# Optimization experiments

Hardware: AMD Instinct MI355X
Metric: run time of the kernel (lower is better)

Reference implementation:

```python
import jax, jax.numpy as jnp
import numpy as np

EPS = 1e-5  # BatchNorm2d default eps


def _conv3x3(x, w):
    # x: [B,C,H,W], w: [O,I,3,3], stride 1, padding 1, no bias
    return jax.lax.conv_general_dilated(
        x, w, window_strides=(1, 1), padding=((1, 1), (1, 1)),
        dimension_numbers=("NCHW", "OIHW", "NCHW"))


def setup_inputs() -> dict:
    key = jax.random.key(0)
    k1, k2, k3 = jax.random.split(key, 3)
    B, C, H, W = 4, 64, 24, 24
    x = jax.random.normal(k1, (B, C, H, W), dtype=jnp.float32)
    gamma = jnp.ones((C,), dtype=jnp.float32)
    beta = jnp.zeros((C,), dtype=jnp.float32)
    # fan-based init scale as in the custom Conv2d (scale=1 and scale=1e-6)
    fan_qkv = (C + 3 * C) / 2 * 9
    bound_qkv = np.sqrt(3.0 / fan_qkv)
    w_qkv = jax.random.uniform(k2, (3 * C, C, 3, 3), minval=-bound_qkv,
                               maxval=bound_qkv, dtype=jnp.float32)
    fan_out = (C + C) / 2 * 9
    bound_out = np.sqrt(3.0 * 1e-6 / fan_out)
    w_out = jax.random.uniform(k3, (C, C, 3, 3), minval=-bound_out,
                               maxval=bound_out, dtype=jnp.float32)
    return {"x": x, "gamma": gamma, "beta": beta, "w_qkv": w_qkv, "w_out": w_out}


def reference(x, gamma, beta, w_qkv, w_out):
    B, C, H, W = x.shape
    # BatchNorm2d (training-mode batch statistics, biased variance)
    mean = jnp.mean(x, axis=(0, 2, 3), keepdims=True)
    var = jnp.var(x, axis=(0, 2, 3), keepdims=True)
    xn = (x - mean) * jax.lax.rsqrt(var + EPS)
    xn = xn * gamma[None, :, None, None] + beta[None, :, None, None]
    qkv = _conv3x3(xn, w_qkv)            # [B,3C,H,W]
    q, k, v = jnp.split(qkv, 3, axis=1)  # each [B,C,H,W]
    scale = 1.0 / np.sqrt(C)
    # per-channel attention: head_dim=1, heads=C
    logits = jnp.einsum("bcyx,bchw->bcyxhw", q, k) * scale  # [B,C,H,W,H,W]
    attn = jax.nn.softmax(logits.reshape(B, C, H, W, H * W), axis=-1)
    attn = attn.reshape(B, C, H, W, H, W)
    out_v = jnp.einsum("bcyxhw,bchw->bcyx", attn, v)  # [B,C,H,W]
    return x + _conv3x3(out_v, w_out)
```

## Files before the change

kernel.cpp:

```cpp
#include <hip/hip_runtime.h>
#include <math.h>

#define B_SZ 4
#define C_IN 64
#define HW_ 576
#define PPLANE 728
#define XH_N   (B_SZ * 32 * PPLANE)

typedef _Float16 h2 __attribute__((ext_vector_type(2)));
typedef _Float16 h8 __attribute__((ext_vector_type(8)));

static __device__ __forceinline__ float dot2(h2 a, h2 b, float c) {
#if __has_builtin(__builtin_amdgcn_fdot2)
  return __builtin_amdgcn_fdot2(a, b, c, false);
#else
  return c + (float)a.x * (float)b.x + (float)a.y * (float)b.y;
#endif
}

static __device__ __forceinline__ float frcp(float d) {
#if __has_builtin(__builtin_amdgcn_rcpf)
  return __builtin_amdgcn_rcpf(d);
#else
  return 1.0f / d;
#endif
}

__global__ __launch_bounds__(256)
void stats_pack_kernel(const float* __restrict__ x, const float* __restrict__ gamma,
                       const float* __restrict__ beta, h2* __restrict__ xh) {
  const int bid = blockIdx.x, tid = threadIdx.x;
  const int icp = bid & 31, b = bid >> 5;
  __shared__ float rs[4], rss[4], ab[4];
  const int c = icp * 2 + (tid >> 7);
  float s = 0.f, ss = 0.f;
  for (int i = (tid & 127); i < B_SZ * HW_; i += 128) {
    int b2 = i / HW_, px = i - b2 * HW_;
    float v = x[(b2 * C_IN + c) * HW_ + px];
    s += v; ss = fmaf(v, v, ss);
  }
#pragma unroll
  for (int off = 32; off > 0; off >>= 1) {
    s += __shfl_down(s, off); ss += __shfl_down(ss, off);
  }
  if ((tid & 63) == 0) { rs[tid >> 6] = s; rss[tid >> 6] = ss; }
  __syncthreads();
  if (tid < 2) {
    float S = rs[tid * 2] + rs[tid * 2 + 1], SS = rss[tid * 2] + rss[tid * 2 + 1];
    const float inv_n = 1.f / (B_SZ * HW_);
    float mean = S * inv_n;
    float var  = SS * inv_n - mean * mean;
    float a = rsqrtf(var + 1e-5f) * gamma[icp * 2 + tid];
    ab[tid * 2] = a;
    ab[tid * 2 + 1] = fmaf(-mean, a, beta[icp * 2 + tid]);
  }
  __syncthreads();
  const float a0 = ab[0], b0 = ab[1], a1 = ab[2], b1 = ab[3];
  h2* plane = xh + (size_t)(b * 32 + icp) * PPLANE;
  const float* src0 = x + (size_t)(b * C_IN + icp * 2) * HW_;
  for (int e = tid; e < PPLANE; e += 256) {
    int rrow = e / 28, ecol = e - rrow * 28;
    int yy = rrow - 1, xx = ecol - 1;
    float f0 = 0.f, f1 = 0.f;
    if ((unsigned)yy < 24u && (unsigned)xx < 24u) {
      f0 = fmaf(src0[yy * 24 + xx],       a0, b0);
      f1 = fmaf(src0[HW_ + yy * 24 + xx], a1, b1);
    }
    h2 v; v.x = (_Float16)f0; v.y = (_Float16)f1;
    plane[e] = v;
  }
}

__global__ __launch_bounds__(576)
void qkv_attn_kernel(const h2* __restrict__ xh, const float* __restrict__ wq,
                     h2* __restrict__ outv) {
  const int bid = blockIdx.x, tid = threadIdx.x;
  const int b = bid >> 6, c = bid & 63;
  const int sub = tid / 144;
  const int r = tid - sub * 144;
  const int y = r / 6, x0 = (r % 6) * 4;

  __shared__ __align__(16) char smem[43424];
  h2*    Wl  = (h2*)smem;
  float* cb  = (float*)(smem + 4096);
  float2* kvs = (float2*)(smem + 24832);
  float* qs  = (float*)(smem + 29440);
  float* red = (float*)(smem + 31744);
  float* FGf = (float*)(smem + 31824);
  float* red2 = (float*)(smem + 31904);

  for (int j = tid; j < 864; j += 576) {
    int icp = j / 27, rem = j - icp * 27;
    int o = rem / 9, t = rem - o * 9;
    int oc = c + 64 * o;
    h2 v;
    v.x = (_Float16)wq[(oc * C_IN + 2 * icp) * 9 + t];
    v.y = (_Float16)wq[(oc * C_IN + 2 * icp + 1) * 9 + t];
    Wl[icp * 32 + rem] = v;
  }
  __syncthreads();

  float acc[3][4] = {{0.f,0.f,0.f,0.f},{0.f,0.f,0.f,0.f},{0.f,0.f,0.f,0.f}};
  const int icp0 = sub * 8;
  const h2* dbase = xh + ((size_t)(b * 32 + icp0) * PPLANE + y * 28 + x0);
#pragma unroll
  for (int i = 0; i < 8; ++i) {
    const h2* dp = dbase + i * PPLANE;
    union { h8 v8[2]; h2 v2[8]; } R0, R1, R2;
    R0.v8[0] = *(const h8*)(dp);      R0.v8[1] = *(const h8*)(dp + 4);
    R1.v8[0] = *(const h8*)(dp + 28); R1.v8[1] = *(const h8*)(dp + 32);
    R2.v8[0] = *(const h8*)(dp + 56); R2.v8[1] = *(const h8*)(dp + 60);
    const h2* wrow = Wl + (icp0 + i) * 32;
    union { h8 v8[7]; h2 v2[28]; } W;
#pragma unroll
    for (int j8 = 0; j8 < 7; ++j8) W.v8[j8] = *(const h8*)(wrow + j8 * 4);
#pragma unroll
    for (int o = 0; o < 3; ++o) {
#pragma unroll
      for (int p = 0; p < 4; ++p) {
        float a = acc[o][p];
        a = dot2(R0.v2[p + 0], W.v2[o * 9 + 0], a);
        a = dot2(R0.v2[p + 1], W.v2[o * 9 + 1], a);
        a = dot2(R0.v2[p + 2], W.v2[o * 9 + 2], a);
        a = dot2(R1.v2[p + 0], W.v2[o * 9 + 3], a);
        a = dot2(R1.v2[p + 1], W.v2[o * 9 + 4], a);
        a = dot2(R1.v2[p + 2], W.v2[o * 9 + 5], a);
        a = dot2(R2.v2[p + 0], W.v2[o * 9 + 6], a);
        a = dot2(R2.v2[p + 1], W.v2[o * 9 + 7], a);
        a = dot2(R2.v2[p + 2], W.v2[o * 9 + 8], a);
        acc[o][p] = a;
      }
    }
  }
  __syncthreads();
  if (sub != 0) {
    const int base = (sub - 1) * 3 * 576;
#pragma unroll
    for (int o = 0; o < 3; ++o)
#pragma unroll
      for (int p = 0; p < 4; ++p)
        cb[base + o * 576 + r * 4 + p] = acc[o][p];
  }
  __syncthreads();
  const float scale_l2e = 0.125f * 1.44269504088896341f;
  if (sub == 0) {
#pragma unroll
    for (int p = 0; p < 4; ++p) {
      float qv = acc[0][p] + cb[0 * 576 + r * 4 + p]
               + cb[3 * 576 + r * 4 + p] + cb[6 * 576 + r * 4 + p];
      float kv = acc[1][p] + cb[1 * 576 + r * 4 + p]
               + cb[4 * 576 + r * 4 + p] + cb[7 * 576 + r * 4 + p];
      float vv = acc[2][p] + cb[2 * 576 + r * 4 + p]
               + cb[5 * 576 + r * 4 + p] + cb[8 * 576 + r * 4 + p];
      qs[4 * r + p] = qv * scale_l2e;
      kvs[4 * r + p] = make_float2(kv, vv);
    }
  }
  __syncthreads();

  const float s = qs[tid];
  float smax = s, smin = s;
#pragma unroll
  for (int off = 32; off > 0; off >>= 1) {
    smax = fmaxf(smax, __shfl_down(smax, off));
    smin = fminf(smin, __shfl_down(smin, off));
  }
  const int wid = tid >> 6;
  if ((tid & 63) == 0) { red[wid] = smax; red[10 + wid] = smin; }
  __syncthreads();
  smax = red[0]; smin = red[10];
#pragma unroll
  for (int w = 1; w < 9; ++w) {
    smax = fmaxf(smax, red[w]); smin = fminf(smin, red[10 + w]);
  }
  const float cc = 0.5f * (smax + smin);
  const float rr = fmaxf(0.5f * (smax - smin), 1e-6f);
  const float COS[9] = { 0.98480775f,  0.86602540f,  0.64278761f,  0.34202014f, 0.f,
                        -0.34202014f, -0.64278761f, -0.86602540f, -0.98480775f };
  const float WJ[9]  = { 0.17364818f, -0.5f,  0.76604444f, -0.93969262f, 1.f,
                        -0.93969262f, 0.76604444f, -0.5f, 0.17364818f };
  float xj[9];
#pragma unroll
  for (int j = 0; j < 9; ++j) xj[j] = fmaf(rr, COS[j], cc);

  const float kk = kvs[tid].x, vv = kvs[tid].y;
  float fj[9], gj[9];
#pragma unroll
  for (int j = 0; j < 9; ++j) {
    float E = __builtin_amdgcn_exp2f(xj[j] * kk);
    gj[j] = E; fj[j] = E * vv;
  }
#pragma unroll
  for (int j = 0; j < 9; ++j) {
    fj[j] += __shfl_xor(fj[j], 1); gj[j] += __shfl_xor(gj[j], 1);
    fj[j] += __shfl_xor(fj[j], 2); gj[j] += __shfl_xor(gj[j], 2);
  }
  if ((tid & 3) == 0) {
    const int row = tid >> 2;
#pragma unroll
    for (int j = 0; j < 9; ++j) {
      red2[row * 20 + j] = fj[j];
      red2[row * 20 + 9 + j] = gj[j];
    }
  }
  __syncthreads();
  if (tid < 144) {
    const int j = tid >> 3, chunk = tid & 7;
    float sum = 0.f;
#pragma unroll
    for (int i = 0; i < 18; ++i) sum += red2[(chunk + 8 * i) * 20 + j];
    sum += __shfl_xor(sum, 1);
    sum += __shfl_xor(sum, 2);
    sum += __shfl_xor(sum, 4);
    if (chunk == 0) FGf[j] = sum;
  }
  __syncthreads();

  float num = 0.f, den = 0.f;
#pragma unroll
  for (int j = 0; j < 9; ++j) {
    float d = s - xj[j];
    d = copysignf(fmaxf(fabsf(d), 1e-7f), d);
    float mu = WJ[j] * frcp(d);
    num = fmaf(mu, FGf[j], num);
    den = fmaf(mu, FGf[9 + j], den);
  }
  float outval = num / den;

  const int icp = c >> 1, hc = c & 1;
  _Float16* plane = reinterpret_cast<_Float16*>(outv + ((size_t)(b * 32) + icp) * PPLANE);
  const int yy = tid / 24, xx = tid - yy * 24;
  plane[((yy + 1) * 28 + (xx + 1)) * 2 + hc] = (_Float16)outval;
  if (tid < 100) {
    int rrow, e;
    if (tid < 26)      { rrow = 0;            e = tid; }
    else if (tid < 52) { rrow = 25;           e = tid - 26; }
    else if (tid < 76) { rrow = tid - 52 + 1; e = 0; }
    else               { rrow = tid - 76 + 1; e = 25; }
    plane[(rrow * 28 + e) * 2 + hc] = (_Float16)0.f;
  }
}

__global__ __launch_bounds__(576)
void conv_out_kernel(const h2* __restrict__ outv, const float* __restrict__ wo,
                     const float* __restrict__ x, float* __restrict__ out) {
  const int bid = blockIdx.x, tid = threadIdx.x;
  const int b = bid >> 6, oc = bid & 63;
  const int sub = tid / 144;
  const int r = tid - sub * 144;
  const int y = r / 6, x0 = (r % 6) * 4;

  __shared__ __align__(16) char smem[8960];
  h2*    Wl = (h2*)smem;
  float* cb = (float*)(smem + 2048);

  for (int j = tid; j < 288; j += 576) {
    int icp = j / 9, t = j - icp * 9;
    h2 v;
    v.x = (_Float16)(wo[(oc * C_IN + 2 * icp) * 9 + t] * 4096.f);
    v.y = (_Float16)(wo[(oc * C_IN + 2 * icp + 1) * 9 + t] * 4096.f);
    Wl[icp * 16 + t] = v;
  }
  __syncthreads();

  float acc[4] = {0.f, 0.f, 0.f, 0.f};
  const int icp0 = sub * 8;
  const h2* dbase = outv + ((size_t)(b * 32 + icp0) * PPLANE + y * 28 + x0);
#pragma unroll
  for (int i = 0; i < 8; ++i) {
    const h2* dp = dbase + i * PPLANE;
    union { h8 v8[2]; h2 v2[8]; } R0, R1, R2;
    R0.v8[0] = *(const h8*)(dp);      R0.v8[1] = *(const h8*)(dp + 4);
    R1.v8[0] = *(const h8*)(dp + 28); R1.v8[1] = *(const h8*)(dp + 32);
    R2.v8[0] = *(const h8*)(dp + 56); R2.v8[1] = *(const h8*)(dp + 60);
    const h2* wrow = Wl + (icp0 + i) * 16;
    union { h8 v8[3]; h2 v2[12]; } W;
    W.v8[0] = *(const h8*)(wrow);
    W.v8[1] = *(const h8*)(wrow + 4);
    W.v8[2] = *(const h8*)(wrow + 8);
#pragma unroll
    for (int p = 0; p < 4; ++p) {
      float a = acc[p];
      a = dot2(R0.v2[p + 0], W.v2[0], a);
      a = dot2(R0.v2[p + 1], W.v2[1], a);
      a = dot2(R0.v2[p + 2], W.v2[2], a);
      a = dot2(R1.v2[p + 0], W.v2[3], a);
      a = dot2(R1.v2[p + 1], W.v2[4], a);
      a = dot2(R1.v2[p + 2], W.v2[5], a);
      a = dot2(R2.v2[p + 0], W.v2[6], a);
      a = dot2(R2.v2[p + 1], W.v2[7], a);
      a = dot2(R2.v2[p + 2], W.v2[8], a);
      acc[p] = a;
    }
  }
  __syncthreads();
  if (sub != 0) {
    const int base = ((sub - 1) * 144 + r) * 4;
#pragma unroll
    for (int p = 0; p < 4; ++p) cb[base + p] = acc[p];
  }
  __syncthreads();
  if (sub == 0) {
    size_t idx = ((size_t)(b * C_IN + oc) * HW_) + 4 * r;
    float4 xr = *reinterpret_cast<const float4*>(x + idx);
    const float inv = 1.f / 4096.f;
    float4 v;
    v.x = fmaf(acc[0] + cb[(0 * 144 + r) * 4 + 0] + cb[(1 * 144 + r) * 4 + 0] + cb[(2 * 144 + r) * 4 + 0], inv, xr.x);
    v.y = fmaf(acc[1] + cb[(0 * 144 + r) * 4 + 1] + cb[(1 * 144 + r) * 4 + 1] + cb[(2 * 144 + r) * 4 + 1], inv, xr.y);
    v.z = fmaf(acc[2] + cb[(0 * 144 + r) * 4 + 2] + cb[(1 * 144 + r) * 4 + 2] + cb[(2 * 144 + r) * 4 + 2], inv, xr.z);
    v.w = fmaf(acc[3] + cb[(0 * 144 + r) * 4 + 3] + cb[(1 * 144 + r) * 4 + 3] + cb[(2 * 144 + r) * 4 + 3], inv, xr.w);
    *reinterpret_cast<float4*>(out + idx) = v;
  }
}

extern "C" void kernel_launch(void* const* d_in, const int* in_sizes, int n_in,
                              void* d_out, int out_size, void* d_ws, size_t ws_size,
                              hipStream_t stream) {
  const float* x     = (const float*)d_in[0];
  const float* gamma = (const float*)d_in[1];
  const float* beta  = (const float*)d_in[2];
  const float* w_qkv = (const float*)d_in[3];
  const float* w_out = (const float*)d_in[4];
  float* out = (float*)d_out;

  h2* xh   = (h2*)d_ws;
  h2* outv = xh + XH_N;

  stats_pack_kernel<<<128, 256, 0, stream>>>(x, gamma, beta, xh);
  qkv_attn_kernel<<<256, 576, 0, stream>>>(xh, w_qkv, outv);
  conv_out_kernel<<<256, 576, 0, stream>>>(outv, w_out, x, out);
}
```

Baseline: 26.45 us.

## Split conv input-channel reduction across seven thread groups with 1024-thread blocks

Both conv kernels move from 576-thread blocks that split input channels four ways (8 pairs each) to 1024-thread blocks where seven 144-thread groups handle 5 or 4 channel pairs. The eighth group's threads only pad the block and are masked out of the attention stage. The first input tile is now prefetched before the weight-staging barrier so its load latency overlaps weight conversion. This shortens each thread's serial dot-product chain. In exchange it adds a larger shared-memory partial-sum reduction, idle threads, and higher register pressure under the 1024-thread launch bound.

```diff
diff --git a/kernel.cpp b/kernel.cpp
--- a/kernel.cpp
+++ b/kernel.cpp
@@ -71,7 +71,7 @@
   }
 }
 
-__global__ __launch_bounds__(576)
+__global__ __launch_bounds__(1024)
 void qkv_attn_kernel(const h2* __restrict__ xh, const float* __restrict__ wq,
                      h2* __restrict__ outv) {
   const int bid = blockIdx.x, tid = threadIdx.x;
@@ -79,18 +79,28 @@
   const int sub = tid / 144;
   const int r = tid - sub * 144;
   const int y = r / 6, x0 = (r % 6) * 4;
-
-  __shared__ __align__(16) char smem[43424];
+  const bool act = sub < 7;
+
+  __shared__ __align__(16) char smem[52656];
   h2*    Wl  = (h2*)smem;
   float* cb  = (float*)(smem + 4096);
-  float2* kvs = (float2*)(smem + 24832);
-  float* qs  = (float*)(smem + 29440);
-  float* red = (float*)(smem + 31744);
-  float* FGf = (float*)(smem + 31824);
-  float* red2 = (float*)(smem + 31904);
-
-  for (int j = tid; j < 864; j += 576) {
-    int icp = j / 27, rem = j - icp * 27;
+  float* red2 = (float*)(smem + 4096);
+  float2* kvs = (float2*)(smem + 45568);
+  float* qs  = (float*)(smem + 50176);
+  float* red = (float*)(smem + 52480);
+  float* FGf = (float*)(smem + 52560);
+
+  const int icp0 = (sub < 4) ? sub * 5 : 20 + (sub - 4) * 4;
+  const int myN  = (sub < 4) ? 5 : 4;
+  const h2* dbase = xh + ((size_t)(b * 32 + (act ? icp0 : 0)) * PPLANE + y * 28 + x0);
+
+  h8 pre[6];
+  pre[0] = *(const h8*)(dbase);      pre[1] = *(const h8*)(dbase + 4);
+  pre[2] = *(const h8*)(dbase + 28); pre[3] = *(const h8*)(dbase + 32);
+  pre[4] = *(const h8*)(dbase + 56); pre[5] = *(const h8*)(dbase + 60);
+
+  if (tid < 864) {
+    int icp = tid / 27, rem = tid - icp * 27;
     int o = rem / 9, t = rem - o * 9;
     int oc = c + 64 * o;
     h2 v;
@@ -101,39 +111,47 @@
   __syncthreads();
 
   float acc[3][4] = {{0.f,0.f,0.f,0.f},{0.f,0.f,0.f,0.f},{0.f,0.f,0.f,0.f}};
-  const int icp0 = sub * 8;
-  const h2* dbase = xh + ((size_t)(b * 32 + icp0) * PPLANE + y * 28 + x0);
-#pragma unroll
-  for (int i = 0; i < 8; ++i) {
-    const h2* dp = dbase + i * PPLANE;
-    union { h8 v8[2]; h2 v2[8]; } R0, R1, R2;
-    R0.v8[0] = *(const h8*)(dp);      R0.v8[1] = *(const h8*)(dp + 4);
-    R1.v8[0] = *(const h8*)(dp + 28); R1.v8[1] = *(const h8*)(dp + 32);
-    R2.v8[0] = *(const h8*)(dp + 56); R2.v8[1] = *(const h8*)(dp + 60);
-    const h2* wrow = Wl + (icp0 + i) * 32;
-    union { h8 v8[7]; h2 v2[28]; } W;
-#pragma unroll
-    for (int j8 = 0; j8 < 7; ++j8) W.v8[j8] = *(const h8*)(wrow + j8 * 4);
-#pragma unroll
-    for (int o = 0; o < 3; ++o) {
-#pragma unroll
-      for (int p = 0; p < 4; ++p) {
-        float a = acc[o][p];
-        a = dot2(R0.v2[p + 0], W.v2[o * 9 + 0], a);
-        a = dot2(R0.v2[p + 1], W.v2[o * 9 + 1], a);
-        a = dot2(R0.v2[p + 2], W.v2[o * 9 + 2], a);
-        a = dot2(R1.v2[p + 0], W.v2[o * 9 + 3], a);
-        a = dot2(R1.v2[p + 1], W.v2[o * 9 + 4], a);
-        a = dot2(R1.v2[p + 2], W.v2[o * 9 + 5], a);
-        a = dot2(R2.v2[p + 0], W.v2[o * 9 + 6], a);
-        a = dot2(R2.v2[p + 1], W.v2[o * 9 + 7], a);
-        a = dot2(R2.v2[p + 2], W.v2[o * 9 + 8], a);
-        acc[o][p] = a;
+  if (act) {
+#pragma unroll
+    for (int i = 0; i < 5; ++i) {
+      if (i < myN) {
+        union { h8 v8[2]; h2 v2[8]; } R0, R1, R2;
+        if (i == 0) {
+          R0.v8[0] = pre[0]; R0.v8[1] = pre[1];
+          R1.v8[0] = pre[2]; R1.v8[1] = pre[3];
+          R2.v8[0] = pre[4]; R2.v8[1] = pre[5];
+        } else {
+          const h2* dp = dbase + i * PPLANE;
+          R0.v8[0] = *(const h8*)(dp);      R0.v8[1] = *(const h8*)(dp + 4);
+          R1.v8[0] = *(const h8*)(dp + 28); R1.v8[1] = *(const h8*)(dp + 32);
+          R2.v8[0] = *(const h8*)(dp + 56); R2.v8[1] = *(const h8*)(dp + 60);
+        }
+        const h2* wrow = Wl + (icp0 + i) * 32;
+        union { h8 v8[7]; h2 v2[28]; } W;
+#pragma unroll
+        for (int j8 = 0; j8 < 7; ++j8) W.v8[j8] = *(const h8*)(wrow + j8 * 4);
+#pragma unroll
+        for (int o = 0; o < 3; ++o) {
+#pragma unroll
+          for (int p = 0; p < 4; ++p) {
+            float a = acc[o][p];
+            a = dot2(R0.v2[p + 0], W.v2[o * 9 + 0], a);
+            a = dot2(R0.v2[p + 1], W.v2[o * 9 + 1], a);
+            a = dot2(R0.v2[p + 2], W.v2[o * 9 + 2], a);
+            a = dot2(R1.v2[p + 0], W.v2[o * 9 + 3], a);
+            a = dot2(R1.v2[p + 1], W.v2[o * 9 + 4], a);
+            a = dot2(R1.v2[p + 2], W.v2[o * 9 + 5], a);
+            a = dot2(R2.v2[p + 0], W.v2[o * 9 + 6], a);
+            a = dot2(R2.v2[p + 1], W.v2[o * 9 + 7], a);
+            a = dot2(R2.v2[p + 2], W.v2[o * 9 + 8], a);
+            acc[o][p] = a;
+          }
+        }
       }
     }
   }
   __syncthreads();
-  if (sub != 0) {
+  if (act && sub != 0) {
     const int base = (sub - 1) * 3 * 576;
 #pragma unroll
     for (int o = 0; o < 3; ++o)
@@ -146,27 +164,29 @@
   if (sub == 0) {
 #pragma unroll
     for (int p = 0; p < 4; ++p) {
-      float qv = acc[0][p] + cb[0 * 576 + r * 4 + p]
-               + cb[3 * 576 + r * 4 + p] + cb[6 * 576 + r * 4 + p];
-      float kv = acc[1][p] + cb[1 * 576 + r * 4 + p]
-               + cb[4 * 576 + r * 4 + p] + cb[7 * 576 + r * 4 + p];
-      float vv = acc[2][p] + cb[2 * 576 + r * 4 + p]
-               + cb[5 * 576 + r * 4 + p] + cb[8 * 576 + r * 4 + p];
+      float qv = acc[0][p], kv = acc[1][p], vv = acc[2][p];
+#pragma unroll
+      for (int s6 = 0; s6 < 6; ++s6) {
+        qv += cb[s6 * 1728 + 0 * 576 + r * 4 + p];
+        kv += cb[s6 * 1728 + 1 * 576 + r * 4 + p];
+        vv += cb[s6 * 1728 + 2 * 576 + r * 4 + p];
+      }
       qs[4 * r + p] = qv * scale_l2e;
       kvs[4 * r + p] = make_float2(kv, vv);
     }
   }
   __syncthreads();
 
-  const float s = qs[tid];
-  float smax = s, smin = s;
+  const bool apx = tid < HW_;
+  const float s = apx ? qs[tid] : 0.f;
+  float smax = apx ? s : -1e30f, smin = apx ? s : 1e30f;
 #pragma unroll
   for (int off = 32; off > 0; off >>= 1) {
     smax = fmaxf(smax, __shfl_down(smax, off));
     smin = fminf(smin, __shfl_down(smin, off));
   }
   const int wid = tid >> 6;
-  if ((tid & 63) == 0) { red[wid] = smax; red[10 + wid] = smin; }
+  if ((tid & 63) == 0 && apx) { red[wid] = smax; red[10 + wid] = smin; }
   __syncthreads();
   smax = red[0]; smin = red[10];
 #pragma unroll
@@ -183,19 +203,22 @@
 #pragma unroll
   for (int j = 0; j < 9; ++j) xj[j] = fmaf(rr, COS[j], cc);
 
-  const float kk = kvs[tid].x, vv = kvs[tid].y;
   float fj[9], gj[9];
-#pragma unroll
-  for (int j = 0; j < 9; ++j) {
-    float E = __builtin_amdgcn_exp2f(xj[j] * kk);
-    gj[j] = E; fj[j] = E * vv;
+  {
+    const float kk = apx ? kvs[tid].x : 0.f;
+    const float vv = apx ? kvs[tid].y : 0.f;
+#pragma unroll
+    for (int j = 0; j < 9; ++j) {
+      float E = apx ? __builtin_amdgcn_exp2f(xj[j] * kk) : 0.f;
+      gj[j] = E; fj[j] = E * vv;
+    }
   }
 #pragma unroll
   for (int j = 0; j < 9; ++j) {
     fj[j] += __shfl_xor(fj[j], 1); gj[j] += __shfl_xor(gj[j], 1);
     fj[j] += __shfl_xor(fj[j], 2); gj[j] += __shfl_xor(gj[j], 2);
   }
-  if ((tid & 3) == 0) {
+  if ((tid & 3) == 0 && apx) {
     const int row = tid >> 2;
 #pragma unroll
     for (int j = 0; j < 9; ++j) {
@@ -216,32 +239,34 @@
   }
   __syncthreads();
 
-  float num = 0.f, den = 0.f;
-#pragma unroll
-  for (int j = 0; j < 9; ++j) {
-    float d = s - xj[j];
-    d = copysignf(fmaxf(fabsf(d), 1e-7f), d);
-    float mu = WJ[j] * frcp(d);
-    num = fmaf(mu, FGf[j], num);
-    den = fmaf(mu, FGf[9 + j], den);
-  }
-  float outval = num / den;
-
-  const int icp = c >> 1, hc = c & 1;
-  _Float16* plane = reinterpret_cast<_Float16*>(outv + ((size_t)(b * 32) + icp) * PPLANE);
-  const int yy = tid / 24, xx = tid - yy * 24;
-  plane[((yy + 1) * 28 + (xx + 1)) * 2 + hc] = (_Float16)outval;
-  if (tid < 100) {
-    int rrow, e;
-    if (tid < 26)      { rrow = 0;            e = tid; }
-    else if (tid < 52) { rrow = 25;           e = tid - 26; }
-    else if (tid < 76) { rrow = tid - 52 + 1; e = 0; }
-    else               { rrow = tid - 76 + 1; e = 25; }
-    plane[(rrow * 28 + e) * 2 + hc] = (_Float16)0.f;
-  }
-}
-
-__global__ __launch_bounds__(576)
+  if (apx) {
+    float num = 0.f, den = 0.f;
+#pragma unroll
+    for (int j = 0; j < 9; ++j) {
+      float d = s - xj[j];
+      d = copysignf(fmaxf(fabsf(d), 1e-7f), d);
+      float mu = WJ[j] * frcp(d);
+      num = fmaf(mu, FGf[j], num);
+      den = fmaf(mu, FGf[9 + j], den);
+    }
+    float outval = num / den;
+
+    const int icp = c >> 1, hc = c & 1;
+    _Float16* plane = reinterpret_cast<_Float16*>(outv + ((size_t)(b * 32) + icp) * PPLANE);
+    const int yy = tid / 24, xx = tid - yy * 24;
+    plane[((yy + 1) * 28 + (xx + 1)) * 2 + hc] = (_Float16)outval;
+    if (tid < 100) {
+      int rrow, e;
+      if (tid < 26)      { rrow = 0;            e = tid; }
+      else if (tid < 52) { rrow = 25;           e = tid - 26; }
+      else if (tid < 76) { rrow = tid - 52 + 1; e = 0; }
+      else               { rrow = tid - 76 + 1; e = 25; }
+      plane[(rrow * 28 + e) * 2 + hc] = (_Float16)0.f;
+    }
+  }
+}
+
+__global__ __launch_bounds__(1024)
 void conv_out_kernel(const h2* __restrict__ outv, const float* __restrict__ wo,
                      const float* __restrict__ x, float* __restrict__ out) {
   const int bid = blockIdx.x, tid = threadIdx.x;
@@ -249,13 +274,23 @@
   const int sub = tid / 144;
   const int r = tid - sub * 144;
   const int y = r / 6, x0 = (r % 6) * 4;
-
-  __shared__ __align__(16) char smem[8960];
+  const bool act = sub < 7;
+
+  __shared__ __align__(16) char smem[15872];
   h2*    Wl = (h2*)smem;
   float* cb = (float*)(smem + 2048);
 
-  for (int j = tid; j < 288; j += 576) {
-    int icp = j / 9, t = j - icp * 9;
+  const int icp0 = (sub < 4) ? sub * 5 : 20 + (sub - 4) * 4;
+  const int myN  = (sub < 4) ? 5 : 4;
+  const h2* dbase = outv + ((size_t)(b * 32 + (act ? icp0 : 0)) * PPLANE + y * 28 + x0);
+
+  h8 pre[6];
+  pre[0] = *(const h8*)(dbase);      pre[1] = *(const h8*)(dbase + 4);
+  pre[2] = *(const h8*)(dbase + 28); pre[3] = *(const h8*)(dbase + 32);
+  pre[4] = *(const h8*)(dbase + 56); pre[5] = *(const h8*)(dbase + 60);
+
+  if (tid < 288) {
+    int icp = tid / 9, t = tid - icp * 9;
     h2 v;
     v.x = (_Float16)(wo[(oc * C_IN + 2 * icp) * 9 + t] * 4096.f);
     v.y = (_Float16)(wo[(oc * C_IN + 2 * icp + 1) * 9 + t] * 4096.f);
@@ -264,37 +299,45 @@
   __syncthreads();
 
   float acc[4] = {0.f, 0.f, 0.f, 0.f};
-  const int icp0 = sub * 8;
-  const h2* dbase = outv + ((size_t)(b * 32 + icp0) * PPLANE + y * 28 + x0);
-#pragma unroll
-  for (int i = 0; i < 8; ++i) {
-    const h2* dp = dbase + i * PPLANE;
-    union { h8 v8[2]; h2 v2[8]; } R0, R1, R2;
-    R0.v8[0] = *(const h8*)(dp);      R0.v8[1] = *(const h8*)(dp + 4);
-    R1.v8[0] = *(const h8*)(dp + 28); R1.v8[1] = *(const h8*)(dp + 32);
-    R2.v8[0] = *(const h8*)(dp + 56); R2.v8[1] = *(const h8*)(dp + 60);
-    const h2* wrow = Wl + (icp0 + i) * 16;
-    union { h8 v8[3]; h2 v2[12]; } W;
-    W.v8[0] = *(const h8*)(wrow);
-    W.v8[1] = *(const h8*)(wrow + 4);
-    W.v8[2] = *(const h8*)(wrow + 8);
-#pragma unroll
-    for (int p = 0; p < 4; ++p) {
-      float a = acc[p];
-      a = dot2(R0.v2[p + 0], W.v2[0], a);
-      a = dot2(R0.v2[p + 1], W.v2[1], a);
-      a = dot2(R0.v2[p + 2], W.v2[2], a);
-      a = dot2(R1.v2[p + 0], W.v2[3], a);
-      a = dot2(R1.v2[p + 1], W.v2[4], a);
-      a = dot2(R1.v2[p + 2], W.v2[5], a);
-      a = dot2(R2.v2[p + 0], W.v2[6], a);
-      a = dot2(R2.v2[p + 1], W.v2[7], a);
-      a = dot2(R2.v2[p + 2], W.v2[8], a);
-      acc[p] = a;
-    }
-  }
-  __syncthreads();
-  if (sub != 0) {
+  if (act) {
+#pragma unroll
+    for (int i = 0; i < 5; ++i) {
+      if (i < myN) {
+        union { h8 v8[2]; h2 v2[8]; } R0, R1, R2;
+        if (i == 0) {
+          R0.v8[0] = pre[0]; R0.v8[1] = pre[1];
+          R1.v8[0] = pre[2]; R1.v8[1] = pre[3];
+          R2.v8[0] = pre[4]; R2.v8[1] = pre[5];
+        } else {
+          const h2* dp = dbase + i * PPLANE;
+          R0.v8[0] = *(const h8*)(dp);      R0.v8[1] = *(const h8*)(dp + 4);
+          R1.v8[0] = *(const h8*)(dp + 28); R1.v8[1] = *(const h8*)(dp + 32);
+          R2.v8[0] = *(const h8*)(dp + 56); R2.v8[1] = *(const h8*)(dp + 60);
+        }
+        const h2* wrow = Wl + (icp0 + i) * 16;
+        union { h8 v8[3]; h2 v2[12]; } W;
+        W.v8[0] = *(const h8*)(wrow);
+        W.v8[1] = *(const h8*)(wrow + 4);
+        W.v8[2] = *(const h8*)(wrow + 8);
+#pragma unroll
+        for (int p = 0; p < 4; ++p) {
+          float a = acc[p];
+          a = dot2(R0.v2[p + 0], W.v2[0], a);
+          a = dot2(R0.v2[p + 1], W.v2[1], a);
+          a = dot2(R0.v2[p + 2], W.v2[2], a);
+          a = dot2(R1.v2[p + 0], W.v2[3], a);
+          a = dot2(R1.v2[p + 1], W.v2[4], a);
+          a = dot2(R1.v2[p + 2], W.v2[5], a);
+          a = dot2(R2.v2[p + 0], W.v2[6], a);
+          a = dot2(R2.v2[p + 1], W.v2[7], a);
+          a = dot2(R2.v2[p + 2], W.v2[8], a);
+          acc[p] = a;
+        }
+      }
+    }
+  }
+  __syncthreads();
+  if (act && sub != 0) {
     const int base = ((sub - 1) * 144 + r) * 4;
 #pragma unroll
     for (int p = 0; p < 4; ++p) cb[base + p] = acc[p];
@@ -304,11 +347,19 @@
     size_t idx = ((size_t)(b * C_IN + oc) * HW_) + 4 * r;
     float4 xr = *reinterpret_cast<const float4*>(x + idx);
     const float inv = 1.f / 4096.f;
+    float sum[4];
+#pragma unroll
+    for (int p = 0; p < 4; ++p) {
+      float a = acc[p];
+#pragma unroll
+      for (int s6 = 0; s6 < 6; ++s6) a += cb[(s6 * 144 + r) * 4 + p];
+      sum[p] = a;
+    }
     float4 v;
-    v.x = fmaf(acc[0] + cb[(0 * 144 + r) * 4 + 0] + cb[(1 * 144 + r) * 4 + 0] + cb[(2 * 144 + r) * 4 + 0], inv, xr.x);
-    v.y = fmaf(acc[1] + cb[(0 * 144 + r) * 4 + 1] + cb[(1 * 144 + r) * 4 + 1] + cb[(2 * 144 + r) * 4 + 1], inv, xr.y);
-    v.z = fmaf(acc[2] + cb[(0 * 144 + r) * 4 + 2] + cb[(1 * 144 + r) * 4 + 2] + cb[(2 * 144 + r) * 4 + 2], inv, xr.z);
-    v.w = fmaf(acc[3] + cb[(0 * 144 + r) * 4 + 3] + cb[(1 * 144 + r) * 4 + 3] + cb[(2 * 144 + r) * 4 + 3], inv, xr.w);
+    v.x = fmaf(sum[0], inv, xr.x);
+    v.y = fmaf(sum[1], inv, xr.y);
+    v.z = fmaf(sum[2], inv, xr.z);
+    v.w = fmaf(sum[3], inv, xr.w);
     *reinterpret_cast<float4*>(out + idx) = v;
   }
 }
@@ -327,6 +378,6 @@
   h2* outv = xh + XH_N;
 
   stats_pack_kernel<<<128, 256, 0, stream>>>(x, gamma, beta, xh);
-  qkv_attn_kernel<<<256, 576, 0, stream>>>(xh, w_qkv, outv);
-  conv_out_kernel<<<256, 576, 0, stream>>>(outv, w_out, x, out);
-}
+  qkv_attn_kernel<<<256, 1024, 0, stream>>>(xh, w_qkv, outv);
+  conv_out_kernel<<<256, 1024, 0, stream>>>(outv, w_out, x, out);
+}
```

After: 27.13 us. 1.03x slower.

## Vectorize BN stats loads, split pack grid, and restructure node reduction per wave

Applied to the files above, without the earlier changes.

The stats kernel now reads x with float4 loads per batch instead of scalar indexed loads, and the grid doubles to 256 blocks, each packing half of a padded plane. In the attention kernel, the 9-node exp-sum reduction is reorganised so each of the 9 waves handles one interpolation node over all 576 keys with a wave shuffle reduction. This removes the shared-memory red2 staging buffer and one barrier, and cuts shared memory per block. Each block in the doubled stats grid still recomputes the full channel statistics, so that redundant work is duplicated.

```diff
diff --git a/kernel.cpp b/kernel.cpp
--- a/kernel.cpp
+++ b/kernel.cpp
@@ -30,14 +30,20 @@
 void stats_pack_kernel(const float* __restrict__ x, const float* __restrict__ gamma,
                        const float* __restrict__ beta, h2* __restrict__ xh) {
   const int bid = blockIdx.x, tid = threadIdx.x;
-  const int icp = bid & 31, b = bid >> 5;
+  const int icp = bid & 31, b = (bid >> 5) & 3, half = bid >> 7;
   __shared__ float rs[4], rss[4], ab[4];
-  const int c = icp * 2 + (tid >> 7);
+  const int ch = icp * 2 + (tid >> 7);
+  const int lane128 = tid & 127;
   float s = 0.f, ss = 0.f;
-  for (int i = (tid & 127); i < B_SZ * HW_; i += 128) {
-    int b2 = i / HW_, px = i - b2 * HW_;
-    float v = x[(b2 * C_IN + c) * HW_ + px];
-    s += v; ss = fmaf(v, v, ss);
+#pragma unroll
+  for (int b2 = 0; b2 < B_SZ; ++b2) {
+    const float4* src4 = (const float4*)(x + (size_t)(b2 * C_IN + ch) * HW_);
+    for (int i = lane128; i < 144; i += 128) {
+      float4 v = src4[i];
+      s += v.x + v.y + v.z + v.w;
+      ss = fmaf(v.x, v.x, ss); ss = fmaf(v.y, v.y, ss);
+      ss = fmaf(v.z, v.z, ss); ss = fmaf(v.w, v.w, ss);
+    }
   }
 #pragma unroll
   for (int off = 32; off > 0; off >>= 1) {
@@ -58,7 +64,8 @@
   const float a0 = ab[0], b0 = ab[1], a1 = ab[2], b1 = ab[3];
   h2* plane = xh + (size_t)(b * 32 + icp) * PPLANE;
   const float* src0 = x + (size_t)(b * C_IN + icp * 2) * HW_;
-  for (int e = tid; e < PPLANE; e += 256) {
+  const int e0 = half * 364;
+  for (int e = e0 + tid; e < e0 + 364; e += 256) {
     int rrow = e / 28, ecol = e - rrow * 28;
     int yy = rrow - 1, xx = ecol - 1;
     float f0 = 0.f, f1 = 0.f;
@@ -80,14 +87,13 @@
   const int r = tid - sub * 144;
   const int y = r / 6, x0 = (r % 6) * 4;
 
-  __shared__ __align__(16) char smem[43424];
+  __shared__ __align__(16) char smem[31904];
   h2*    Wl  = (h2*)smem;
   float* cb  = (float*)(smem + 4096);
   float2* kvs = (float2*)(smem + 24832);
   float* qs  = (float*)(smem + 29440);
   float* red = (float*)(smem + 31744);
   float* FGf = (float*)(smem + 31824);
-  float* red2 = (float*)(smem + 31904);
 
   for (int j = tid; j < 864; j += 576) {
     int icp = j / 27, rem = j - icp * 27;
@@ -183,36 +189,25 @@
 #pragma unroll
   for (int j = 0; j < 9; ++j) xj[j] = fmaf(rr, COS[j], cc);
 
-  const float kk = kvs[tid].x, vv = kvs[tid].y;
-  float fj[9], gj[9];
-#pragma unroll
-  for (int j = 0; j < 9; ++j) {
-    float E = __builtin_amdgcn_exp2f(xj[j] * kk);
-    gj[j] = E; fj[j] = E * vv;
-  }
-#pragma unroll
-  for (int j = 0; j < 9; ++j) {
-    fj[j] += __shfl_xor(fj[j], 1); gj[j] += __shfl_xor(gj[j], 1);
-    fj[j] += __shfl_xor(fj[j], 2); gj[j] += __shfl_xor(gj[j], 2);
-  }
-  if ((tid & 3) == 0) {
-    const int row = tid >> 2;
-#pragma unroll
-    for (int j = 0; j < 9; ++j) {
-      red2[row * 20 + j] = fj[j];
-      red2[row * 20 + 9 + j] = gj[j];
-    }
-  }
-  __syncthreads();
-  if (tid < 144) {
-    const int j = tid >> 3, chunk = tid & 7;
-    float sum = 0.f;
-#pragma unroll
-    for (int i = 0; i < 18; ++i) sum += red2[(chunk + 8 * i) * 20 + j];
-    sum += __shfl_xor(sum, 1);
-    sum += __shfl_xor(sum, 2);
-    sum += __shfl_xor(sum, 4);
-    if (chunk == 0) FGf[j] = sum;
+  {
+    float xjw = xj[0];
+#pragma unroll
+    for (int j = 1; j < 9; ++j) if (wid == j) xjw = xj[j];
+    const int lane = tid & 63;
+    float fsum = 0.f, gsum = 0.f;
+#pragma unroll
+    for (int i = 0; i < 9; ++i) {
+      float2 kv = kvs[lane + 64 * i];
+      float E = __builtin_amdgcn_exp2f(xjw * kv.x);
+      gsum += E;
+      fsum = fmaf(E, kv.y, fsum);
+    }
+#pragma unroll
+    for (int off = 32; off > 0; off >>= 1) {
+      fsum += __shfl_down(fsum, off);
+      gsum += __shfl_down(gsum, off);
+    }
+    if ((tid & 63) == 0) { FGf[wid] = fsum; FGf[9 + wid] = gsum; }
   }
   __syncthreads();
 
@@ -326,7 +321,7 @@
   h2* xh   = (h2*)d_ws;
   h2* outv = xh + XH_N;
 
-  stats_pack_kernel<<<128, 256, 0, stream>>>(x, gamma, beta, xh);
+  stats_pack_kernel<<<256, 256, 0, stream>>>(x, gamma, beta, xh);
   qkv_attn_kernel<<<256, 576, 0, stream>>>(xh, w_qkv, outv);
   conv_out_kernel<<<256, 576, 0, stream>>>(outv, w_out, x, out);
 }
```

After: 25.63 us. 3.1% less time.
